# Performance work log

Hardware: AMD Instinct MI355X
Metric: run time of the kernel (lower is better)

Reference implementation:

```python
import jax, jax.numpy as jnp
import numpy as np

N_HEADS = 16
NEG_INF = float('-inf')


def setup_inputs() -> dict:
    key = jax.random.key(0)
    ks = jax.random.split(key, 8)
    B, S, D = 8, 1024, 1024
    inp = {
        'q': jax.random.normal(ks[0], (B, S, D), jnp.float32),
        'k': jax.random.normal(ks[1], (B, S, D), jnp.float32),
        'v': jax.random.normal(ks[2], (B, S, D), jnp.float32),
        'key_padding_mask': jnp.zeros((B, S), bool),
        'Wq': jax.random.normal(ks[3], (D, D), jnp.float32) / np.sqrt(D),
        'bq': jnp.zeros((D,), jnp.float32),
        'Wk': jax.random.normal(ks[4], (D, D), jnp.float32) / np.sqrt(D),
        'bk': jnp.zeros((D,), jnp.float32),
        'Wv': jax.random.normal(ks[5], (D, D), jnp.float32) / np.sqrt(D),
        'bv': jnp.zeros((D,), jnp.float32),
        'Wo': jax.random.normal(ks[6], (D, D), jnp.float32) / np.sqrt(D),
        'bo': jnp.zeros((D,), jnp.float32),
    }
    return inp


def reference(q, k, v, key_padding_mask, Wq, bq, Wk, bk, Wv, bv, Wo, bo):
    B, T, D = q.shape
    S = k.shape[1]
    H = N_HEADS
    dh = D // H
    causal = True

    # projections (torch Linear: x @ W.T + b)
    qh = (q @ Wq.T + bq).reshape(B, T, H, dh).transpose(0, 2, 1, 3)  # b h t d
    kh = (k @ Wk.T + bk).reshape(B, S, H, dh).transpose(0, 2, 1, 3)  # b h s d
    vh = (v @ Wv.T + bv).reshape(B, S, H, dh).transpose(0, 2, 1, 3)  # b h s d

    s = jnp.einsum('bhtd,bhsd->bhts', qh, kh) / jnp.sqrt(jnp.asarray(dh, s_dtype(qh)))
    s = jnp.where(key_padding_mask[:, None, None, :], NEG_INF, s)
    if causal:
        cmask = jnp.triu(jnp.full((T, S), NEG_INF, s.dtype), 1)
        s = s + cmask[None, None]
    a = jax.nn.softmax(s.astype(jnp.float32), axis=-1).astype(s.dtype)
    o = jnp.einsum('bhts,bhsd->bhtd', a, vh)
    o = o.transpose(0, 2, 1, 3).reshape(B, T, D)
    return o @ Wo.T + bo


def s_dtype(x):
    return x.dtype
```

## Files before the change

### kernel.cpp

```cpp
#include <hip/hip_runtime.h>
#include <hip/hip_bf16.h>

typedef unsigned short u16;
typedef unsigned int u32;
typedef __attribute__((ext_vector_type(8))) short bf16x8;
typedef __attribute__((ext_vector_type(4))) float f32x4;

#define LOG2E 1.44269504088896340736f
#define QSCALE (0.125f * LOG2E)


__device__ inline u16 f2bf(float f) {
  union { float f; u32 u; } v; v.f = f;
  u32 r = v.u + 0x7fffu + ((v.u >> 16) & 1u);
  return (u16)(r >> 16);
}
__device__ inline u16 f2bf_fast(float f) {
  u32 u = __builtin_bit_cast(u32, f);
  return (u16)((u + 0x8000u) >> 16);
}

__device__ inline void gload_lds16(const u16* g, u16* l) {
  __builtin_amdgcn_global_load_lds(
      (const __attribute__((address_space(1))) u32*)g,
      (__attribute__((address_space(3))) u32*)l, 16, 0, 0);
}

template<int CTRL>
__device__ inline float dppmov(float x) {
  int i = __builtin_bit_cast(int, x);
  int r = __builtin_amdgcn_update_dpp(i, i, CTRL, 0xf, 0xf, false);
  return __builtin_bit_cast(float, r);
}
__device__ inline float rowmax16(float v) {
  v = fmaxf(v, dppmov<0x128>(v));
  v = fmaxf(v, dppmov<0x124>(v));
  v = fmaxf(v, dppmov<0x122>(v));
  v = fmaxf(v, dppmov<0x121>(v));
  return v;
}
__device__ inline float rowsum16(float v) {
  v += dppmov<0x128>(v);
  v += dppmov<0x124>(v);
  v += dppmov<0x122>(v);
  v += dppmov<0x121>(v);
  return v;
}


__global__ void cvt_multi(const float4* __restrict__ s0, const float4* __restrict__ s1,
                          const float4* __restrict__ s2, const float4* __restrict__ s3,
                          ushort4* __restrict__ d0, ushort4* __restrict__ d1,
                          ushort4* __restrict__ d2, ushort4* __restrict__ d3, int n4) {
  const float4* s; ushort4* d;
  switch (blockIdx.y) {
    case 0: s = s0; d = d0; break;
    case 1: s = s1; d = d1; break;
    case 2: s = s2; d = d2; break;
    default: s = s3; d = d3; break;
  }
  int stride = gridDim.x * blockDim.x;
  for (int i = blockIdx.x * blockDim.x + threadIdx.x; i < n4; i += stride) {
    float4 v = s[i];
    ushort4 o;
    o.x = f2bf(v.x); o.y = f2bf(v.y); o.z = f2bf(v.z); o.w = f2bf(v.w);
    d[i] = o;
  }
}


__global__ void mask_flags(const unsigned char* __restrict__ mask,
                           unsigned char* __restrict__ flags) {
  int t = threadIdx.x;
  if (t >= 128) return;
  const uint4* p = (const uint4*)(mask + (size_t)t * 64);
  uint4 a = p[0], b = p[1], c = p[2], d = p[3];
  u32 v = a.x | a.y | a.z | a.w | b.x | b.y | b.z | b.w |
          c.x | c.y | c.z | c.w | d.x | d.y | d.z | d.w;
  flags[t] = v ? 1 : 0;
}


__global__ __launch_bounds__(256) void gemm_qkv_f32a(
    const float* __restrict__ Aqf, const float* __restrict__ Akf, const float* __restrict__ Avf,
    const u16* __restrict__ Wqb, const u16* __restrict__ Wkb, const u16* __restrict__ Wvb,
    const float* __restrict__ bqp, const float* __restrict__ bkp, const float* __restrict__ bvp,
    u16* __restrict__ Qh, u16* __restrict__ Kh, u16* __restrict__ Vt,
    int M, int N, int K) {
  constexpr int BK = 32;
  __shared__ u16 sA[2][128 * BK];
  __shared__ u16 sB[2][128 * BK];

  const int nx = gridDim.x;
  const int nxy = gridDim.x * gridDim.y;
  const int nwg = nxy * gridDim.z;
  const int hw = blockIdx.z * nxy + blockIdx.y * nx + blockIdx.x;
  const int per = nwg >> 3;
  const int lg = (hw & 7) * per + (hw >> 3);
  const int z = lg / nxy;
  const int rem = lg - z * nxy;
  const int m0 = (rem >> 3) * 128;
  const int n0 = (rem & 7) * 128;

  const float* Af = (z == 0) ? Aqf : (z == 1) ? Akf : Avf;
  const u16* Bt   = (z == 0) ? Wqb : (z == 1) ? Wkb : Wvb;
  const float* bias = (z == 0) ? bqp : (z == 1) ? bkp : bvp;

  const int tid = threadIdx.x;
  const int lane = tid & 63;
  const int wave = tid >> 6;
  const int g = lane >> 4;
  const int r = lane & 15;
  const int wr = wave >> 1, wc = wave & 1;

  f32x4 acc[4][4] = {};
  float4 areg0, areg1, areg2, areg3;

  const int c0 = tid, c1 = tid + 256;
  const int row0 = c0 >> 2, cc0 = c0 & 3;
  const int row1 = c1 >> 2, cc1 = c1 & 3;

  auto loadA = [&](int kt) {
    const int k0 = kt * BK;
    const float* p0 = Af + (size_t)(m0 + row0) * K + k0 + cc0 * 8;
    const float* p1 = Af + (size_t)(m0 + row1) * K + k0 + cc1 * 8;
    areg0 = *(const float4*)(p0);
    areg1 = *(const float4*)(p0 + 4);
    areg2 = *(const float4*)(p1);
    areg3 = *(const float4*)(p1 + 4);
  };
  auto writeA = [&](int buf) {
    bf16x8 pk0, pk1;
    pk0[0] = (short)f2bf_fast(areg0.x); pk0[1] = (short)f2bf_fast(areg0.y);
    pk0[2] = (short)f2bf_fast(areg0.z); pk0[3] = (short)f2bf_fast(areg0.w);
    pk0[4] = (short)f2bf_fast(areg1.x); pk0[5] = (short)f2bf_fast(areg1.y);
    pk0[6] = (short)f2bf_fast(areg1.z); pk0[7] = (short)f2bf_fast(areg1.w);
    pk1[0] = (short)f2bf_fast(areg2.x); pk1[1] = (short)f2bf_fast(areg2.y);
    pk1[2] = (short)f2bf_fast(areg2.z); pk1[3] = (short)f2bf_fast(areg2.w);
    pk1[4] = (short)f2bf_fast(areg3.x); pk1[5] = (short)f2bf_fast(areg3.y);
    pk1[6] = (short)f2bf_fast(areg3.z); pk1[7] = (short)f2bf_fast(areg3.w);
    *(bf16x8*)(&sA[buf][c0 * 8]) = pk0;
    *(bf16x8*)(&sA[buf][c1 * 8]) = pk1;
  };
  auto stageB = [&](int buf, int kt) {
    const int k0 = kt * BK;
#pragma unroll
    for (int i = 0; i < 2; ++i) {
      int c = tid + i * 256;
      int rw = c >> 2, cc = c & 3;
      gload_lds16(Bt + (size_t)(n0 + rw) * K + k0 + cc * 8, &sB[buf][0] + c * 8);
    }
  };

  stageB(0, 0);
  loadA(0);
  writeA(0);

  const int NT = K / BK;
  for (int kt = 0; kt < NT; ++kt) {
    __syncthreads();
    const int nxt = (kt + 1) & 1;
    if (kt + 1 < NT) {
      stageB(nxt, kt + 1);
      loadA(kt + 1);
    }
    const u16* a_base = &sA[kt & 1][0];
    const u16* b_base = &sB[kt & 1][0];
    bf16x8 avf[4], bvf[4];
#pragma unroll
    for (int i = 0; i < 4; ++i) {
      avf[i] = *(const bf16x8*)(a_base + (wr * 64 + i * 16 + r) * BK + g * 8);
      bvf[i] = *(const bf16x8*)(b_base + (wc * 64 + i * 16 + r) * BK + g * 8);
    }
#pragma unroll
    for (int i = 0; i < 4; ++i)
#pragma unroll
      for (int j = 0; j < 4; ++j)
        acc[i][j] = __builtin_amdgcn_mfma_f32_16x16x32_bf16(avf[i], bvf[j], acc[i][j], 0, 0, 0);
    if (kt + 1 < NT) writeA(nxt);
  }

#pragma unroll
  for (int i = 0; i < 4; ++i) {
    int rowb = m0 + wr * 64 + i * 16 + g * 4;
#pragma unroll
    for (int j = 0; j < 4; ++j) {
      int col = n0 + wc * 64 + j * 16 + r;
      float bv = bias[col];
#pragma unroll
      for (int q = 0; q < 4; ++q) {
        int row = rowb + q;
        float v = acc[i][j][q] + bv;
        int b = row >> 10, t = row & 1023, h = col >> 6, d = col & 63;
        if (z == 0) {
          Qh[((((size_t)b * 16 + h) << 10) + t) * 64 + d] = f2bf(v * QSCALE);
        } else if (z == 1) {
          Kh[((((size_t)b * 16 + h) << 10) + t) * 64 + d] = f2bf(v);
        } else {
          Vt[(((size_t)b * 16 + h) * 64 + d) * 1024 + t] = f2bf(v);
        }
      }
    }
  }
}


__global__ __launch_bounds__(256) void gemm_o(
    const u16* __restrict__ A, const u16* __restrict__ Bt,
    const float* __restrict__ bias, float* __restrict__ Cout,
    int M, int N, int K) {
  constexpr int BK = 32;
  __shared__ u16 sA[2][128 * BK];
  __shared__ u16 sB[2][128 * BK];

  const int nx = gridDim.x;
  const int nwg = gridDim.x * gridDim.y;
  const int hw = blockIdx.y * nx + blockIdx.x;
  const int per = nwg >> 3;
  const int lg = (hw & 7) * per + (hw >> 3);
  const int m0 = (lg >> 3) * 128;
  const int n0 = (lg & 7) * 128;

  const int tid = threadIdx.x;
  const int lane = tid & 63;
  const int wave = tid >> 6;
  const int g = lane >> 4;
  const int r = lane & 15;
  const int wr = wave >> 1, wc = wave & 1;

  f32x4 acc[4][4] = {};

  auto stage = [&](int buf, int kt) {
    const int k0 = kt * BK;
#pragma unroll
    for (int i = 0; i < 2; ++i) {
      int c = tid + i * 256;
      int row = c >> 2, cc = c & 3;
      gload_lds16(A + (size_t)(m0 + row) * K + k0 + cc * 8, &sA[buf][0] + c * 8);
    }
#pragma unroll
    for (int i = 0; i < 2; ++i) {
      int c = tid + i * 256;
      int row = c >> 2, cc = c & 3;
      gload_lds16(Bt + (size_t)(n0 + row) * K + k0 + cc * 8, &sB[buf][0] + c * 8);
    }
  };

  stage(0, 0);
  const int NT = K / BK;
  for (int kt = 0; kt < NT; ++kt) {
    __syncthreads();
    if (kt + 1 < NT) stage((kt + 1) & 1, kt + 1);
    const u16* a_base = &sA[kt & 1][0];
    const u16* b_base = &sB[kt & 1][0];
    bf16x8 avf[4], bvf[4];
#pragma unroll
    for (int i = 0; i < 4; ++i) {
      avf[i] = *(const bf16x8*)(a_base + (wr * 64 + i * 16 + r) * BK + g * 8);
      bvf[i] = *(const bf16x8*)(b_base + (wc * 64 + i * 16 + r) * BK + g * 8);
    }
#pragma unroll
    for (int i = 0; i < 4; ++i)
#pragma unroll
      for (int j = 0; j < 4; ++j)
        acc[i][j] = __builtin_amdgcn_mfma_f32_16x16x32_bf16(avf[i], bvf[j], acc[i][j], 0, 0, 0);
  }

#pragma unroll
  for (int i = 0; i < 4; ++i) {
    int rowb = m0 + wr * 64 + i * 16 + g * 4;
#pragma unroll
    for (int j = 0; j < 4; ++j) {
      int col = n0 + wc * 64 + j * 16 + r;
      float bv = bias[col];
#pragma unroll
      for (int q = 0; q < 4; ++q) {
        int row = rowb + q;
        Cout[(size_t)row * N + col] = acc[i][j][q] + bv;
      }
    }
  }
}


__global__ __launch_bounds__(256) void attn_fwd(
    const u16* __restrict__ Qh, const u16* __restrict__ Kh,
    const u16* __restrict__ Vt, const unsigned char* __restrict__ mask,
    const unsigned char* __restrict__ padflags,
    u16* __restrict__ O) {
  constexpr int S = 1024, DH = 64;
  __shared__ u16 sK[2][64 * 64];
  __shared__ u16 sV[2][64 * 64];
  __shared__ u16 sP[4][16 * 64];

  const int tid = threadIdx.x, lane = tid & 63, wave = tid >> 6;
  const int g = lane >> 4, r = lane & 15;
  const int bh = blockIdx.x;
  const int qt = (int)gridDim.y - 1 - (int)blockIdx.y;
  const int b = bh >> 4, h = bh & 15;
  const int qw = qt * 128 + wave * 32;

  bf16x8 qf[2][2];
#pragma unroll
  for (int u = 0; u < 2; ++u) {
    const u16* Qb = Qh + ((size_t)bh * S + qw + u * 16 + r) * DH;
    qf[u][0] = *(const bf16x8*)(Qb + g * 8);
    qf[u][1] = *(const bf16x8*)(Qb + 32 + g * 8);
  }

  f32x4 acc[2][4] = {};
  float mrun[2][4], lrun[2][4];
#pragma unroll
  for (int u = 0; u < 2; ++u)
#pragma unroll
    for (int i = 0; i < 4; ++i) { mrun[u][i] = -INFINITY; lrun[u][i] = 0.f; }

  auto stage = [&](int buf, int kvt) {
    const int s0k = kvt * 64;
#pragma unroll
    for (int i = 0; i < 2; ++i) {
      int c = tid + i * 256;
      int row = c >> 3;
      int cc = (c & 7) ^ (row & 7);
      gload_lds16(Kh + ((size_t)bh * S + s0k + row) * DH + cc * 8, &sK[buf][0] + c * 8);
      gload_lds16(Vt + ((size_t)bh * DH + row) * S + s0k + cc * 8, &sV[buf][0] + c * 8);
    }
  };

  const int NT = 2 * (qt + 1);
  stage(0, 0);
  for (int kvt = 0; kvt < NT; ++kvt) {
    __syncthreads();
    if (kvt + 1 < NT) stage((kvt + 1) & 1, kvt + 1);
    const int cur = kvt & 1;
    const int s0 = kvt * 64;
    const bool pad = padflags[b * 16 + (s0 >> 6)] != 0;
    const u16* Kb = &sK[cur][0];
    const u16* Vb = &sV[cur][0];
    u16* Pw = &sP[wave][0];

#pragma unroll
    for (int u = 0; u < 2; ++u) {
      const int qg = qw + u * 16;
      if (s0 > qg + 15) continue;
      const bool diag = (s0 + 63 > qg);

      f32x4 sc[4] = {};
#pragma unroll
      for (int ss = 0; ss < 4; ++ss) {
#pragma unroll
        for (int kc = 0; kc < 2; ++kc) {
          int krow = ss * 16 + r;
          int byteoff = krow * 128 + kc * 64 + g * 16;
          bf16x8 kf = *(const bf16x8*)((const char*)Kb + (byteoff ^ ((krow & 7) << 4)));
          sc[ss] = __builtin_amdgcn_mfma_f32_16x16x32_bf16(qf[u][kc], kf, sc[ss], 0, 0, 0);
        }
      }

      float sv[4][4];
      float pmax[4] = {-INFINITY, -INFINITY, -INFINITY, -INFINITY};
#pragma unroll
      for (int ss = 0; ss < 4; ++ss) {
        float padd = 0.f;
        if (pad) {
          int s_g = s0 + ss * 16 + r;
          if (mask[(size_t)b * S + s_g]) padd = -INFINITY;
        }
#pragma unroll
        for (int reg = 0; reg < 4; ++reg) {
          float v = sc[ss][reg] + padd;
          if (diag) {
            int s_g = s0 + ss * 16 + r;
            int q_g = qg + g * 4 + reg;
            if (s_g > q_g) v = -INFINITY;
          }
          sv[ss][reg] = v;
          pmax[reg] = fmaxf(pmax[reg], v);
        }
      }
#pragma unroll
      for (int reg = 0; reg < 4; ++reg) {
        float m = rowmax16(pmax[reg]);
        float newm = fmaxf(mrun[u][reg], m);
        float alpha = (newm == -INFINITY) ? 1.f : exp2f(mrun[u][reg] - newm);
        mrun[u][reg] = newm;
        float rs = 0.f;
#pragma unroll
        for (int ss = 0; ss < 4; ++ss) {
          float p = (newm == -INFINITY) ? 0.f : exp2f(sv[ss][reg] - newm);
          sv[ss][reg] = p;
          rs += p;
        }
        rs = rowsum16(rs);
        lrun[u][reg] = lrun[u][reg] * alpha + rs;
#pragma unroll
        for (int df = 0; df < 4; ++df) acc[u][df][reg] *= alpha;
      }

#pragma unroll
      for (int ss = 0; ss < 4; ++ss) {
#pragma unroll
        for (int reg = 0; reg < 4; ++reg) {
          int qrow = g * 4 + reg;
          int byteoff = qrow * 128 + (ss * 16 + r) * 2;
          u32 bits = __builtin_bit_cast(u32, sv[ss][reg]);
          *(u16*)((char*)Pw + (byteoff ^ ((qrow & 7) << 4))) = (u16)(bits >> 16);
        }
      }

#pragma unroll
      for (int sc2 = 0; sc2 < 2; ++sc2) {
        int pbyte = r * 128 + sc2 * 64 + g * 16;
        bf16x8 pf = *(const bf16x8*)((const char*)Pw + (pbyte ^ ((r & 7) << 4)));
#pragma unroll
        for (int df = 0; df < 4; ++df) {
          int vrow = df * 16 + r;
          int vbyte = vrow * 128 + sc2 * 64 + g * 16;
          bf16x8 vf = *(const bf16x8*)((const char*)Vb + (vbyte ^ ((vrow & 7) << 4)));
          acc[u][df] = __builtin_amdgcn_mfma_f32_16x16x32_bf16(pf, vf, acc[u][df], 0, 0, 0);
        }
      }
    }
  }

#pragma unroll
  for (int u = 0; u < 2; ++u) {
#pragma unroll
    for (int reg = 0; reg < 4; ++reg) {
      float l = lrun[u][reg];
      float inv = (l > 0.f) ? 1.f / l : 0.f;
      int t = qw + u * 16 + g * 4 + reg;
#pragma unroll
      for (int df = 0; df < 4; ++df) {
        float vo = acc[u][df][reg] * inv;
        O[((size_t)b * 1024 + t) * 1024 + h * 64 + df * 16 + r] = f2bf(vo);
      }
    }
  }
}


extern "C" void kernel_launch(void* const* d_in, const int* in_sizes, int n_in,
                              void* d_out, int out_size, void* d_ws, size_t ws_size,
                              hipStream_t stream) {
  const float* q  = (const float*)d_in[0];
  const float* k  = (const float*)d_in[1];
  const float* v  = (const float*)d_in[2];
  const unsigned char* mask = (const unsigned char*)d_in[3];
  const float* Wq = (const float*)d_in[4];
  const float* bq = (const float*)d_in[5];
  const float* Wk = (const float*)d_in[6];
  const float* bk = (const float*)d_in[7];
  const float* Wv = (const float*)d_in[8];
  const float* bv = (const float*)d_in[9];
  const float* Wo = (const float*)d_in[10];
  const float* bo = (const float*)d_in[11];

  const int M = 8192, N = 1024, K = 1024;
  const size_t MB = 1u << 20;
  char* ws = (char*)d_ws;

  u16* AttO = (u16*)(ws);
  u16* Qh   = (u16*)(ws + 16 * MB);
  u16* Kh   = (u16*)(ws + 32 * MB);
  u16* Vt   = (u16*)(ws + 48 * MB);
  u16* Wqb  = (u16*)(ws + 64 * MB);
  u16* Wkb  = Wqb + (1u << 20);
  u16* Wvb  = Wkb + (1u << 20);
  u16* Wob  = Wvb + (1u << 20);
  unsigned char* flags = (unsigned char*)(ws + 72 * MB);

  cvt_multi<<<dim3(256, 4), 256, 0, stream>>>(
      (const float4*)Wq, (const float4*)Wk, (const float4*)Wv, (const float4*)Wo,
      (ushort4*)Wqb, (ushort4*)Wkb, (ushort4*)Wvb, (ushort4*)Wob, (N * K) / 4);
  mask_flags<<<1, 128, 0, stream>>>(mask, flags);

  gemm_qkv_f32a<<<dim3(N / 128, M / 128, 3), 256, 0, stream>>>(
      q, k, v, Wqb, Wkb, Wvb, bq, bk, bv, Qh, Kh, Vt, M, N, K);

  attn_fwd<<<dim3(128, 8), 256, 0, stream>>>(Qh, Kh, Vt, mask, flags, AttO);

  gemm_o<<<dim3(N / 128, M / 128), 256, 0, stream>>>(
      AttO, Wob, bo, (float*)d_out, M, N, K);
}
```

Baseline: 217.0 us.

## Stage fp32 A tiles via direct-to-LDS loads and XOR-swizzle LDS tiles

The QKV projection GEMM now copies fp32 activation tiles straight into shared memory with global_load_lds and converts them to bf16 at fragment-read time using byte permutes (truncation, not rounding). This replaces the register round trip and the manual bf16 pack and store. Both GEMM kernels also XOR-swizzle their LDS tile layouts to reduce bank conflicts on the fragment reads. The cost is twice the LDS footprint for the A tile, extra permute instructions per fragment, and slightly different bf16 rounding.

```diff
diff --git a/kernel.cpp b/kernel.cpp
--- a/kernel.cpp
+++ b/kernel.cpp
@@ -5,6 +5,7 @@
 typedef unsigned int u32;
 typedef __attribute__((ext_vector_type(8))) short bf16x8;
 typedef __attribute__((ext_vector_type(4))) float f32x4;
+typedef __attribute__((ext_vector_type(4))) unsigned int u32x4v;
 
 #define LOG2E 1.44269504088896340736f
 #define QSCALE (0.125f * LOG2E)
@@ -15,12 +16,8 @@
   u32 r = v.u + 0x7fffu + ((v.u >> 16) & 1u);
   return (u16)(r >> 16);
 }
-__device__ inline u16 f2bf_fast(float f) {
-  u32 u = __builtin_bit_cast(u32, f);
-  return (u16)((u + 0x8000u) >> 16);
-}
-
-__device__ inline void gload_lds16(const u16* g, u16* l) {
+
+__device__ inline void gload_lds16(const void* g, void* l) {
   __builtin_amdgcn_global_load_lds(
       (const __attribute__((address_space(1))) u32*)g,
       (__attribute__((address_space(3))) u32*)l, 16, 0, 0);
@@ -88,8 +85,8 @@
     u16* __restrict__ Qh, u16* __restrict__ Kh, u16* __restrict__ Vt,
     int M, int N, int K) {
   constexpr int BK = 32;
-  __shared__ u16 sA[2][128 * BK];
-  __shared__ u16 sB[2][128 * BK];
+  __shared__ float sAf[2][128 * BK];
+  __shared__ u16   sB [2][128 * BK];
 
   const int nx = gridDim.x;
   const int nxy = gridDim.x * gridDim.y;
@@ -114,70 +111,60 @@
   const int wr = wave >> 1, wc = wave & 1;
 
   f32x4 acc[4][4] = {};
-  float4 areg0, areg1, areg2, areg3;
-
-  const int c0 = tid, c1 = tid + 256;
-  const int row0 = c0 >> 2, cc0 = c0 & 3;
-  const int row1 = c1 >> 2, cc1 = c1 & 3;
-
-  auto loadA = [&](int kt) {
+
+  auto stage = [&](int buf, int kt) {
     const int k0 = kt * BK;
-    const float* p0 = Af + (size_t)(m0 + row0) * K + k0 + cc0 * 8;
-    const float* p1 = Af + (size_t)(m0 + row1) * K + k0 + cc1 * 8;
-    areg0 = *(const float4*)(p0);
-    areg1 = *(const float4*)(p0 + 4);
-    areg2 = *(const float4*)(p1);
-    areg3 = *(const float4*)(p1 + 4);
-  };
-  auto writeA = [&](int buf) {
-    bf16x8 pk0, pk1;
-    pk0[0] = (short)f2bf_fast(areg0.x); pk0[1] = (short)f2bf_fast(areg0.y);
-    pk0[2] = (short)f2bf_fast(areg0.z); pk0[3] = (short)f2bf_fast(areg0.w);
-    pk0[4] = (short)f2bf_fast(areg1.x); pk0[5] = (short)f2bf_fast(areg1.y);
-    pk0[6] = (short)f2bf_fast(areg1.z); pk0[7] = (short)f2bf_fast(areg1.w);
-    pk1[0] = (short)f2bf_fast(areg2.x); pk1[1] = (short)f2bf_fast(areg2.y);
-    pk1[2] = (short)f2bf_fast(areg2.z); pk1[3] = (short)f2bf_fast(areg2.w);
-    pk1[4] = (short)f2bf_fast(areg3.x); pk1[5] = (short)f2bf_fast(areg3.y);
-    pk1[6] = (short)f2bf_fast(areg3.z); pk1[7] = (short)f2bf_fast(areg3.w);
-    *(bf16x8*)(&sA[buf][c0 * 8]) = pk0;
-    *(bf16x8*)(&sA[buf][c1 * 8]) = pk1;
-  };
-  auto stageB = [&](int buf, int kt) {
-    const int k0 = kt * BK;
+#pragma unroll
+    for (int i = 0; i < 4; ++i) {
+      int c = tid + i * 256;
+      int row = c >> 3, cc = c & 7;
+      int scc = cc ^ (row & 7);
+      gload_lds16(Af + (size_t)(m0 + row) * K + k0 + scc * 4,
+                  (char*)&sAf[buf][0] + c * 16);
+    }
 #pragma unroll
     for (int i = 0; i < 2; ++i) {
       int c = tid + i * 256;
-      int rw = c >> 2, cc = c & 3;
-      gload_lds16(Bt + (size_t)(n0 + rw) * K + k0 + cc * 8, &sB[buf][0] + c * 8);
+      int row = c >> 2, cc = c & 3;
+      int scc = cc ^ ((row >> 1) & 3);
+      gload_lds16(Bt + (size_t)(n0 + row) * K + k0 + scc * 8,
+                  (char*)&sB[buf][0] + c * 16);
     }
   };
 
-  stageB(0, 0);
-  loadA(0);
-  writeA(0);
-
+  auto compute = [&](int buf) {
+    const char* aB = (const char*)&sAf[buf][0];
+    const char* bB = (const char*)&sB[buf][0];
+    bf16x8 avf[4], bvf[4];
+#pragma unroll
+    for (int i = 0; i < 4; ++i) {
+      int arow = wr * 64 + i * 16 + r;
+      const char* rb = aB + arow * 128;
+      int s7 = arow & 7;
+      uint4 q0 = *(const uint4*)(rb + (((g * 2)     ^ s7) * 16));
+      uint4 q1 = *(const uint4*)(rb + (((g * 2 + 1) ^ s7) * 16));
+      u32x4v w;
+      w.x = __builtin_amdgcn_perm(q0.y, q0.x, 0x07060302u);
+      w.y = __builtin_amdgcn_perm(q0.w, q0.z, 0x07060302u);
+      w.z = __builtin_amdgcn_perm(q1.y, q1.x, 0x07060302u);
+      w.w = __builtin_amdgcn_perm(q1.w, q1.z, 0x07060302u);
+      avf[i] = __builtin_bit_cast(bf16x8, w);
+      int brow = wc * 64 + i * 16 + r;
+      bvf[i] = *(const bf16x8*)(bB + brow * 64 + ((g ^ ((brow >> 1) & 3)) * 16));
+    }
+#pragma unroll
+    for (int i = 0; i < 4; ++i)
+#pragma unroll
+      for (int j = 0; j < 4; ++j)
+        acc[i][j] = __builtin_amdgcn_mfma_f32_16x16x32_bf16(avf[i], bvf[j], acc[i][j], 0, 0, 0);
+  };
+
+  stage(0, 0);
   const int NT = K / BK;
   for (int kt = 0; kt < NT; ++kt) {
     __syncthreads();
-    const int nxt = (kt + 1) & 1;
-    if (kt + 1 < NT) {
-      stageB(nxt, kt + 1);
-      loadA(kt + 1);
-    }
-    const u16* a_base = &sA[kt & 1][0];
-    const u16* b_base = &sB[kt & 1][0];
-    bf16x8 avf[4], bvf[4];
-#pragma unroll
-    for (int i = 0; i < 4; ++i) {
-      avf[i] = *(const bf16x8*)(a_base + (wr * 64 + i * 16 + r) * BK + g * 8);
-      bvf[i] = *(const bf16x8*)(b_base + (wc * 64 + i * 16 + r) * BK + g * 8);
-    }
-#pragma unroll
-    for (int i = 0; i < 4; ++i)
-#pragma unroll
-      for (int j = 0; j < 4; ++j)
-        acc[i][j] = __builtin_amdgcn_mfma_f32_16x16x32_bf16(avf[i], bvf[j], acc[i][j], 0, 0, 0);
-    if (kt + 1 < NT) writeA(nxt);
+    if (kt + 1 < NT) stage((kt + 1) & 1, kt + 1);
+    compute(kt & 1);
   }
 
 #pragma unroll
@@ -236,13 +223,17 @@
     for (int i = 0; i < 2; ++i) {
       int c = tid + i * 256;
       int row = c >> 2, cc = c & 3;
-      gload_lds16(A + (size_t)(m0 + row) * K + k0 + cc * 8, &sA[buf][0] + c * 8);
+      int scc = cc ^ ((row >> 1) & 3);
+      gload_lds16(A + (size_t)(m0 + row) * K + k0 + scc * 8,
+                  (char*)&sA[buf][0] + c * 16);
     }
 #pragma unroll
     for (int i = 0; i < 2; ++i) {
       int c = tid + i * 256;
       int row = c >> 2, cc = c & 3;
-      gload_lds16(Bt + (size_t)(n0 + row) * K + k0 + cc * 8, &sB[buf][0] + c * 8);
+      int scc = cc ^ ((row >> 1) & 3);
+      gload_lds16(Bt + (size_t)(n0 + row) * K + k0 + scc * 8,
+                  (char*)&sB[buf][0] + c * 16);
     }
   };
 
@@ -251,13 +242,15 @@
   for (int kt = 0; kt < NT; ++kt) {
     __syncthreads();
     if (kt + 1 < NT) stage((kt + 1) & 1, kt + 1);
-    const u16* a_base = &sA[kt & 1][0];
-    const u16* b_base = &sB[kt & 1][0];
+    const char* aB = (const char*)&sA[kt & 1][0];
+    const char* bB = (const char*)&sB[kt & 1][0];
     bf16x8 avf[4], bvf[4];
 #pragma unroll
     for (int i = 0; i < 4; ++i) {
-      avf[i] = *(const bf16x8*)(a_base + (wr * 64 + i * 16 + r) * BK + g * 8);
-      bvf[i] = *(const bf16x8*)(b_base + (wc * 64 + i * 16 + r) * BK + g * 8);
+      int arow = wr * 64 + i * 16 + r;
+      avf[i] = *(const bf16x8*)(aB + arow * 64 + ((g ^ ((arow >> 1) & 3)) * 16));
+      int brow = wc * 64 + i * 16 + r;
+      bvf[i] = *(const bf16x8*)(bB + brow * 64 + ((g ^ ((brow >> 1) & 3)) * 16));
     }
 #pragma unroll
     for (int i = 0; i < 4; ++i)
```

New measurement: 216.5 us. Within noise of the previous version (-0.2%).
